# Kernel optimization log

Measured on AMD Instinct MI355X. Metric: run time of the kernel, lower is better.

Reference implementation:

```python
import jax, jax.numpy as jnp
import numpy as np

B, C, H, W = 16, 3, 512, 512
NUM_BANDS = 100


def setup_inputs() -> dict:
    key = jax.random.key(0)
    k1, k2, k3 = jax.random.split(key, 3)
    clean = jax.random.normal(k1, (B, C, H, W), dtype=jnp.float32)
    noisy = jax.random.normal(k2, (B, C, H, W), dtype=jnp.float32)
    # value_prob = arange(1.0, 0.0, -0.01) * 0.3, bernoulli per batch row
    probs = (1.0 - 0.01 * jnp.arange(NUM_BANDS, dtype=jnp.float32)) * 0.3  # (100,)
    value_set = jax.random.bernoulli(k3, probs[None, :].repeat(B, axis=0)).astype(jnp.float32)  # (B,100)
    return {"clean": clean, "noisy": noisy, "value_set": value_set}


def reference(clean, noisy, value_set):
    b, c, h, w = noisy.shape
    # radial distance map from image center (meshgrid 'ij' as in torch)
    a = jnp.arange(h, dtype=jnp.float32)[:, None]
    bb = jnp.arange(w, dtype=jnp.float32)[None, :]
    dist = jnp.sqrt((a - h / 2) ** 2 + (bb - w / 2) ** 2)  # (H,W)
    max_radius = float(np.sqrt(h * h + w * w) / 2)
    radius_set = max_radius * jnp.arange(0.01, 1.01, 0.01, dtype=jnp.float32)  # (100,)

    # FFT + full fftshift (torch default shifts ALL axes, incl. batch/channel)
    noisy_fq = jnp.fft.fftshift(jnp.fft.fftn(noisy, axes=(-1, -2)))
    clean_fq = jnp.fft.fftshift(jnp.fft.fftn(clean, axes=(-1, -2)))

    # Fused bucketize + gather replacing the 100-iteration mask loop:
    # band i covers radius_set[i-1] <= dist < radius_set[i]  ->  searchsorted right
    idx = jnp.searchsorted(radius_set, dist, side='right')  # (H,W), values in [0,100]
    in_range = idx < radius_set.shape[0]
    idx_c = jnp.minimum(idx, radius_set.shape[0] - 1)
    bn1_mask = jnp.where(in_range[None, :, :], value_set[:, idx_c], 0.0)  # (B,H,W)
    bn2_mask = 1.0 - bn1_mask

    replaced_fq = noisy_fq * bn1_mask[:, None, :, :] + clean_fq * bn2_mask[:, None, :, :]
    replaced_fq = jnp.fft.ifftshift(replaced_fq)
    out = jnp.fft.ifftn(replaced_fq, axes=(-1, -2))
    return out.real
```

## Files before the change

### kernel.cpp

```cpp
#include <hip/hip_runtime.h>
#include <math.h>


using cplx = float2;

__device__ __forceinline__ cplx cmul(cplx a, cplx b){
  return make_float2(a.x*b.x - a.y*b.y, a.x*b.y + a.y*b.x);
}
__device__ __forceinline__ cplx cadd(cplx a, cplx b){ return make_float2(a.x+b.x, a.y+b.y); }
__device__ __forceinline__ cplx csub(cplx a, cplx b){ return make_float2(a.x-b.x, a.y-b.y); }
template<int S> __device__ __forceinline__ cplx muli(cplx a){
  return (S < 0) ? make_float2(a.y, -a.x) : make_float2(-a.y, a.x);
}
__device__ __forceinline__ int sw(int i){ return i ^ (((i >> 6) & 7) << 1); }

template<int S>
__device__ __forceinline__ void dft8(cplx v[8]){
  const float R2 = 0.70710678118654752440f;
  cplx e0 = cadd(v[0], v[4]), e1 = csub(v[0], v[4]);
  cplx o0 = cadd(v[2], v[6]), o1 = muli<S>(csub(v[2], v[6]));
  cplx E0 = cadd(e0, o0), E1 = cadd(e1, o1), E2 = csub(e0, o0), E3 = csub(e1, o1);
  cplx f0 = cadd(v[1], v[5]), f1 = csub(v[1], v[5]);
  cplx g0 = cadd(v[3], v[7]), g1 = muli<S>(csub(v[3], v[7]));
  cplx F0 = cadd(f0, g0), F1 = cadd(f1, g1), F2 = csub(f0, g0), F3 = csub(f1, g1);
  const cplx w1 = make_float2( R2, (float)S * R2);
  const cplx w3 = make_float2(-R2, (float)S * R2);
  cplx t0 = F0, t1 = cmul(w1, F1), t2 = muli<S>(F2), t3 = cmul(w3, F3);
  v[0] = cadd(E0, t0); v[4] = csub(E0, t0);
  v[1] = cadd(E1, t1); v[5] = csub(E1, t1);
  v[2] = cadd(E2, t2); v[6] = csub(E2, t2);
  v[3] = cadd(E3, t3); v[7] = csub(E3, t3);
}

template<int S>
__device__ __forceinline__ void twiddle8_pair(cplx a[8], cplx b[8], float ang){
  float sn, c_; __sincosf(ang, &sn, &c_);
  cplx w = make_float2(c_, sn), cur = w;
  #pragma unroll
  for(int r = 1; r < 8; r++){ a[r] = cmul(a[r], cur); b[r] = cmul(b[r], cur); cur = cmul(cur, w); }
}

template<int S, int STR>
__device__ __forceinline__ void fft512_pair(cplx a[8], cplx b[8], cplx* sa, cplx* sb, int t){
  const float PI2 = 6.283185307179586f;
  dft8<S>(a); dft8<S>(b);
  #pragma unroll
  for(int r = 0; r < 8; r++){ int i = sw(t*8 + r)*STR; sa[i] = a[r]; sb[i] = b[r]; }
  #pragma unroll
  for(int r = 0; r < 8; r++){ int i = sw(t + 64*r)*STR; a[r] = sa[i]; b[r] = sb[i]; }
  twiddle8_pair<S>(a, b, (float)S * PI2 * (1.0f/64.0f) * (float)(t & 7));
  dft8<S>(a); dft8<S>(b);
  int d1 = ((t >> 3) << 6) | (t & 7);
  #pragma unroll
  for(int r = 0; r < 8; r++){ int i = sw(d1 + (r << 3))*STR; sa[i] = a[r]; sb[i] = b[r]; }
  #pragma unroll
  for(int r = 0; r < 8; r++){ int i = sw(t + 64*r)*STR; a[r] = sa[i]; b[r] = sb[i]; }
  twiddle8_pair<S>(a, b, (float)S * PI2 * (1.0f/512.0f) * (float)t);
  dft8<S>(a); dft8<S>(b);
}

__device__ __forceinline__ void packed_images(int p, int& i0, int& i1, int& b1, int& b2){
  if (p < 16){ i0 = 3*p; i1 = 3*p + 1; b1 = p; b2 = p; }
  else { int q = p - 16; i0 = 6*q + 2; i1 = 6*q + 5; b1 = 2*q; b2 = 2*q + 1; }
}

__device__ __forceinline__ int slot_col(int s, int j){
  int c = (j < 4) ? (4*s + j) : (505 - 4*s + j);
  c &= 511;
  if (s == 0 && j == 7) c = 256;
  return c;
}

__global__ __launch_bounds__(256) void k_rowfft(const float* __restrict__ noisy,
                                                const float* __restrict__ clean,
                                                float2* __restrict__ ws){
  __shared__ cplx scr[8][512];
  int blk = blockIdx.x;
  int p = blk >> 6, h8 = (blk & 63) << 3;
  int i0, i1, b1, b2; packed_images(p, i0, i1, b1, b2);
  const float* n0 = noisy + (size_t)i0 * 262144;
  const float* c0 = clean + (size_t)i0 * 262144;
  const float* n1 = noisy + (size_t)i1 * 262144;
  const float* c1 = clean + (size_t)i1 * 262144;
  int wid = threadIdx.x >> 6, t = threadIdx.x & 63;
  int hA = h8 + wid*2, hB = hA + 1;
  cplx a[8], b[8];
  #pragma unroll
  for(int r = 0; r < 8; r++){
    int iA = hA*512 + t + 64*r;
    int iB = hB*512 + t + 64*r;
    a[r] = make_float2(n0[iA]-c0[iA], n1[iA]-c1[iA]);
    b[r] = make_float2(n0[iB]-c0[iB], n1[iB]-c1[iB]);
  }
  fft512_pair<-1,1>(a, b, scr[wid*2], scr[wid*2+1], t);
  float2* oA = ws + (size_t)p*262144 + hA*512;
  float2* oB = ws + (size_t)p*262144 + hB*512;
  #pragma unroll
  for(int r = 0; r < 8; r++){ oA[t+64*r] = a[r]; oB[t+64*r] = b[r]; }
}

#define INV_BAND 0.27621358640099513f

__global__ __launch_bounds__(256) void k_colfft(float2* __restrict__ ws,
                                                const float* __restrict__ value_set){
  __shared__ cplx tile[512][9];
  int blk = blockIdx.x;
  int p = blk >> 6, s = blk & 63;
  int i0, i1, b1, b2; packed_images(p, i0, i1, b1, b2);
  const float* vs1 = value_set + ((b1 + 8) & 15) * 100;
  const float* vs2 = value_set + ((b2 + 8) & 15) * 100;
  float2* base = ws + (size_t)p * 262144;
  int tid = threadIdx.x;

  {
    int j = tid & 7, cj = slot_col(s, j);
    #pragma unroll
    for(int h0 = 0; h0 < 512; h0 += 32){
      int h = h0 + (tid >> 3);
      tile[h][j] = base[h*512 + cj];
    }
  }
  __syncthreads();

  int wid = tid >> 6, t = tid & 63;
  int sA = wid, sB = 7 - wid;
  int colA = slot_col(s, sA);
  int colB = slot_col(s, sB);
  int fwA = (colA < 256) ? colA : colA - 512;
  int fwB = (colB < 256) ? colB : colB - 512;
  int fw2A = fwA * fwA;
  int fw2B = fwB * fwB;
  bool selfp = (s == 0 && wid == 0);
  int pA = selfp ? sA : sB;
  int pB = selfp ? sB : sA;

  cplx a[8], b[8];
  #pragma unroll
  for(int r = 0; r < 8; r++){ a[r] = tile[t+64*r][sA]; b[r] = tile[t+64*r][sB]; }
  fft512_pair<-1,9>(a, b, &tile[0][sA], &tile[0][sB], t);
  #pragma unroll
  for(int r = 0; r < 8; r++){ tile[t+64*r][sA] = a[r]; tile[t+64*r][sB] = b[r]; }
  #pragma unroll
  for(int r = 0; r < 8; r++){
    int h = t + 64*r;
    int fh = (h < 256) ? h : h - 512;
    int fh2 = fh * fh;
    float rrA = sqrtf((float)(fh2 + fw2A));
    float rrB = sqrtf((float)(fh2 + fw2B));
    int bandA = (int)(rrA * INV_BAND);
    int bandB = (int)(rrB * INV_BAND);
    float m1A = (bandA < 100) ? vs1[bandA] : 0.0f;
    float m2A = (bandA < 100) ? vs2[bandA] : 0.0f;
    float m1B = (bandB < 100) ? vs1[bandB] : 0.0f;
    float m2B = (bandB < 100) ? vs2[bandB] : 0.0f;
    float csA = 0.5f*(m1A + m2A) * (1.0f/262144.0f);
    float cdA = 0.5f*(m1A - m2A) * (1.0f/262144.0f);
    float csB = 0.5f*(m1B + m2B) * (1.0f/262144.0f);
    float cdB = 0.5f*(m1B - m2B) * (1.0f/262144.0f);
    int ph = (512 - h) & 511;
    float2 PA = tile[ph][pA];
    float2 PB = tile[ph][pB];
    cplx na = make_float2(csA*a[r].x + cdA*PA.x, csA*a[r].y - cdA*PA.y);
    cplx nb = make_float2(csB*b[r].x + cdB*PB.x, csB*b[r].y - cdB*PB.y);
    a[r] = na; b[r] = nb;
  }
  fft512_pair<1,9>(a, b, &tile[0][sA], &tile[0][sB], t);
  #pragma unroll
  for(int r = 0; r < 8; r++){ tile[t+64*r][sA] = a[r]; tile[t+64*r][sB] = b[r]; }
  __syncthreads();

  {
    int j = tid & 7, cj = slot_col(s, j);
    #pragma unroll
    for(int h0 = 0; h0 < 512; h0 += 32){
      int h = h0 + (tid >> 3);
      base[h*512 + cj] = tile[h][j];
    }
  }
}

__global__ __launch_bounds__(256) void k_rowifft(const float2* __restrict__ ws,
                                                 const float* __restrict__ clean,
                                                 float* __restrict__ out){
  __shared__ cplx scr[8][512];
  int blk = blockIdx.x;
  int p = blk >> 6, h8 = (blk & 63) << 3;
  int i0, i1, b1, b2; packed_images(p, i0, i1, b1, b2);
  int wid = threadIdx.x >> 6, t = threadIdx.x & 63;
  int hA = h8 + wid*2, hB = hA + 1;
  const float2* iA_ = ws + (size_t)p*262144 + hA*512;
  const float2* iB_ = ws + (size_t)p*262144 + hB*512;
  cplx a[8], b[8];
  #pragma unroll
  for(int r = 0; r < 8; r++){ a[r] = iA_[t+64*r]; b[r] = iB_[t+64*r]; }
  fft512_pair<1,1>(a, b, scr[wid*2], scr[wid*2+1], t);
  const float* c0 = clean + (size_t)i0 * 262144;
  const float* c1 = clean + (size_t)i1 * 262144;
  float* o0 = out + (size_t)i0 * 262144;
  float* o1 = out + (size_t)i1 * 262144;
  #pragma unroll
  for(int r = 0; r < 8; r++){
    int iA = hA*512 + t + 64*r;
    int iB = hB*512 + t + 64*r;
    o0[iA] = a[r].x + c0[iA];
    o1[iA] = a[r].y + c1[iA];
    o0[iB] = b[r].x + c0[iB];
    o1[iB] = b[r].y + c1[iB];
  }
}

extern "C" void kernel_launch(void* const* d_in, const int* in_sizes, int n_in,
                              void* d_out, int out_size, void* d_ws, size_t ws_size,
                              hipStream_t stream){
  const float* clean     = (const float*)d_in[0];
  const float* noisy     = (const float*)d_in[1];
  const float* value_set = (const float*)d_in[2];
  float* out = (float*)d_out;
  float2* ws = (float2*)d_ws;

  k_rowfft <<<1536, 256, 0, stream>>>(noisy, clean, ws);
  k_colfft <<<1536, 256, 0, stream>>>(ws, value_set);
  k_rowifft<<<1536, 256, 0, stream>>>(ws, clean, out);
}
```

Before: 227.8 us.

## Fold conjugate column pairs adjacent in workspace and widen column FFT tiles

The row FFT now writes each row in a folded order, so column w and its conjugate partner 512-w sit next to each other, and the row IFFT reads back with the same mapping. The column kernel can then load 16 contiguous columns per block (512 threads, 768 blocks) instead of gathering 8 scattered columns, which makes the global loads and stores contiguous. The shared tile uses an XOR-swizzled layout to avoid bank conflicts. Packed images from the same batch skip the conjugate-partner read and extra tile store in the mask step. The row kernels also get an occupancy hint in launch_bounds. The change risks higher register pressure in the larger column blocks and a new, more complex index mapping that has to be correct.

```diff
diff --git a/kernel.cpp b/kernel.cpp
--- a/kernel.cpp
+++ b/kernel.cpp
@@ -13,6 +13,11 @@
   return (S < 0) ? make_float2(a.y, -a.x) : make_float2(-a.y, a.x);
 }
 __device__ __forceinline__ int sw(int i){ return i ^ (((i >> 6) & 7) << 1); }
+#define ADDR(i,j) (((i) << 4) + ((j) ^ ((((i) >> 3) ^ (((i) & 7) << 1)) & 15)))
+
+__device__ __forceinline__ int fold(int w){
+  return (w < 256) ? 2*w : ((w == 256) ? 1 : 2*(512 - w) + 1);
+}
 
 template<int S>
 __device__ __forceinline__ void dft8(cplx v[8]){
@@ -40,21 +45,40 @@
   for(int r = 1; r < 8; r++){ a[r] = cmul(a[r], cur); b[r] = cmul(b[r], cur); cur = cmul(cur, w); }
 }
 
-template<int S, int STR>
+template<int S>
 __device__ __forceinline__ void fft512_pair(cplx a[8], cplx b[8], cplx* sa, cplx* sb, int t){
   const float PI2 = 6.283185307179586f;
   dft8<S>(a); dft8<S>(b);
   #pragma unroll
-  for(int r = 0; r < 8; r++){ int i = sw(t*8 + r)*STR; sa[i] = a[r]; sb[i] = b[r]; }
-  #pragma unroll
-  for(int r = 0; r < 8; r++){ int i = sw(t + 64*r)*STR; a[r] = sa[i]; b[r] = sb[i]; }
+  for(int r = 0; r < 8; r++){ int i = sw(t*8 + r); sa[i] = a[r]; sb[i] = b[r]; }
+  #pragma unroll
+  for(int r = 0; r < 8; r++){ int i = sw(t + 64*r); a[r] = sa[i]; b[r] = sb[i]; }
   twiddle8_pair<S>(a, b, (float)S * PI2 * (1.0f/64.0f) * (float)(t & 7));
   dft8<S>(a); dft8<S>(b);
   int d1 = ((t >> 3) << 6) | (t & 7);
   #pragma unroll
-  for(int r = 0; r < 8; r++){ int i = sw(d1 + (r << 3))*STR; sa[i] = a[r]; sb[i] = b[r]; }
-  #pragma unroll
-  for(int r = 0; r < 8; r++){ int i = sw(t + 64*r)*STR; a[r] = sa[i]; b[r] = sb[i]; }
+  for(int r = 0; r < 8; r++){ int i = sw(d1 + (r << 3)); sa[i] = a[r]; sb[i] = b[r]; }
+  #pragma unroll
+  for(int r = 0; r < 8; r++){ int i = sw(t + 64*r); a[r] = sa[i]; b[r] = sb[i]; }
+  twiddle8_pair<S>(a, b, (float)S * PI2 * (1.0f/512.0f) * (float)t);
+  dft8<S>(a); dft8<S>(b);
+}
+
+template<int S>
+__device__ __forceinline__ void fft512_pair_tile(cplx a[8], cplx b[8], cplx* T, int jA, int jB, int t){
+  const float PI2 = 6.283185307179586f;
+  dft8<S>(a); dft8<S>(b);
+  #pragma unroll
+  for(int r = 0; r < 8; r++){ int i = t*8 + r; T[ADDR(i,jA)] = a[r]; T[ADDR(i,jB)] = b[r]; }
+  #pragma unroll
+  for(int r = 0; r < 8; r++){ int i = t + 64*r; a[r] = T[ADDR(i,jA)]; b[r] = T[ADDR(i,jB)]; }
+  twiddle8_pair<S>(a, b, (float)S * PI2 * (1.0f/64.0f) * (float)(t & 7));
+  dft8<S>(a); dft8<S>(b);
+  int d1 = ((t >> 3) << 6) | (t & 7);
+  #pragma unroll
+  for(int r = 0; r < 8; r++){ int i = d1 + (r << 3); T[ADDR(i,jA)] = a[r]; T[ADDR(i,jB)] = b[r]; }
+  #pragma unroll
+  for(int r = 0; r < 8; r++){ int i = t + 64*r; a[r] = T[ADDR(i,jA)]; b[r] = T[ADDR(i,jB)]; }
   twiddle8_pair<S>(a, b, (float)S * PI2 * (1.0f/512.0f) * (float)t);
   dft8<S>(a); dft8<S>(b);
 }
@@ -64,16 +88,9 @@
   else { int q = p - 16; i0 = 6*q + 2; i1 = 6*q + 5; b1 = 2*q; b2 = 2*q + 1; }
 }
 
-__device__ __forceinline__ int slot_col(int s, int j){
-  int c = (j < 4) ? (4*s + j) : (505 - 4*s + j);
-  c &= 511;
-  if (s == 0 && j == 7) c = 256;
-  return c;
-}
-
-__global__ __launch_bounds__(256) void k_rowfft(const float* __restrict__ noisy,
-                                                const float* __restrict__ clean,
-                                                float2* __restrict__ ws){
+__global__ __launch_bounds__(256, 5) void k_rowfft(const float* __restrict__ noisy,
+                                                   const float* __restrict__ clean,
+                                                   float2* __restrict__ ws){
   __shared__ cplx scr[8][512];
   int blk = blockIdx.x;
   int p = blk >> 6, h8 = (blk & 63) << 3;
@@ -92,96 +109,114 @@
     a[r] = make_float2(n0[iA]-c0[iA], n1[iA]-c1[iA]);
     b[r] = make_float2(n0[iB]-c0[iB], n1[iB]-c1[iB]);
   }
-  fft512_pair<-1,1>(a, b, scr[wid*2], scr[wid*2+1], t);
+  fft512_pair<-1>(a, b, scr[wid*2], scr[wid*2+1], t);
   float2* oA = ws + (size_t)p*262144 + hA*512;
   float2* oB = ws + (size_t)p*262144 + hB*512;
   #pragma unroll
-  for(int r = 0; r < 8; r++){ oA[t+64*r] = a[r]; oB[t+64*r] = b[r]; }
+  for(int r = 0; r < 8; r++){
+    int s = fold(t + 64*r);
+    oA[s] = a[r]; oB[s] = b[r];
+  }
 }
 
 #define INV_BAND 0.27621358640099513f
 
-__global__ __launch_bounds__(256) void k_colfft(float2* __restrict__ ws,
+__global__ __launch_bounds__(512) void k_colfft(float2* __restrict__ ws,
                                                 const float* __restrict__ value_set){
-  __shared__ cplx tile[512][9];
+  __shared__ cplx tile[512 * 16];
   int blk = blockIdx.x;
-  int p = blk >> 6, s = blk & 63;
+  int p = blk >> 5, m = blk & 31;
   int i0, i1, b1, b2; packed_images(p, i0, i1, b1, b2);
   const float* vs1 = value_set + ((b1 + 8) & 15) * 100;
   const float* vs2 = value_set + ((b2 + 8) & 15) * 100;
-  float2* base = ws + (size_t)p * 262144;
+  bool cross = (p >= 16);
+  float2* base = ws + (size_t)p * 262144 + 16*m;
   int tid = threadIdx.x;
 
   {
-    int j = tid & 7, cj = slot_col(s, j);
+    int j = tid & 15, hb = tid >> 4;
     #pragma unroll
     for(int h0 = 0; h0 < 512; h0 += 32){
-      int h = h0 + (tid >> 3);
-      tile[h][j] = base[h*512 + cj];
+      int h = h0 + hb;
+      tile[ADDR(h, j)] = base[(size_t)h * 512 + j];
     }
   }
   __syncthreads();
 
   int wid = tid >> 6, t = tid & 63;
-  int sA = wid, sB = 7 - wid;
-  int colA = slot_col(s, sA);
-  int colB = slot_col(s, sB);
-  int fwA = (colA < 256) ? colA : colA - 512;
-  int fwB = (colB < 256) ? colB : colB - 512;
-  int fw2A = fwA * fwA;
-  int fw2B = fwB * fwB;
-  bool selfp = (s == 0 && wid == 0);
-  int pA = selfp ? sA : sB;
-  int pB = selfp ? sB : sA;
+  int jA = wid*2, jB = wid*2 + 1;
+  int SA = 16*m + jA;
+  int wA = SA >> 1;
+  int fw2A = wA * wA;
+  int fw2B = (SA == 0) ? 65536 : wA * wA;
+  bool selfp = (SA == 0);
+  int pjA = selfp ? jA : jB;
+  int pjB = selfp ? jB : jA;
 
   cplx a[8], b[8];
   #pragma unroll
-  for(int r = 0; r < 8; r++){ a[r] = tile[t+64*r][sA]; b[r] = tile[t+64*r][sB]; }
-  fft512_pair<-1,9>(a, b, &tile[0][sA], &tile[0][sB], t);
-  #pragma unroll
-  for(int r = 0; r < 8; r++){ tile[t+64*r][sA] = a[r]; tile[t+64*r][sB] = b[r]; }
-  #pragma unroll
-  for(int r = 0; r < 8; r++){
-    int h = t + 64*r;
-    int fh = (h < 256) ? h : h - 512;
-    int fh2 = fh * fh;
-    float rrA = sqrtf((float)(fh2 + fw2A));
-    float rrB = sqrtf((float)(fh2 + fw2B));
-    int bandA = (int)(rrA * INV_BAND);
-    int bandB = (int)(rrB * INV_BAND);
-    float m1A = (bandA < 100) ? vs1[bandA] : 0.0f;
-    float m2A = (bandA < 100) ? vs2[bandA] : 0.0f;
-    float m1B = (bandB < 100) ? vs1[bandB] : 0.0f;
-    float m2B = (bandB < 100) ? vs2[bandB] : 0.0f;
-    float csA = 0.5f*(m1A + m2A) * (1.0f/262144.0f);
-    float cdA = 0.5f*(m1A - m2A) * (1.0f/262144.0f);
-    float csB = 0.5f*(m1B + m2B) * (1.0f/262144.0f);
-    float cdB = 0.5f*(m1B - m2B) * (1.0f/262144.0f);
-    int ph = (512 - h) & 511;
-    float2 PA = tile[ph][pA];
-    float2 PB = tile[ph][pB];
-    cplx na = make_float2(csA*a[r].x + cdA*PA.x, csA*a[r].y - cdA*PA.y);
-    cplx nb = make_float2(csB*b[r].x + cdB*PB.x, csB*b[r].y - cdB*PB.y);
-    a[r] = na; b[r] = nb;
-  }
-  fft512_pair<1,9>(a, b, &tile[0][sA], &tile[0][sB], t);
-  #pragma unroll
-  for(int r = 0; r < 8; r++){ tile[t+64*r][sA] = a[r]; tile[t+64*r][sB] = b[r]; }
+  for(int r = 0; r < 8; r++){ int i = t + 64*r; a[r] = tile[ADDR(i,jA)]; b[r] = tile[ADDR(i,jB)]; }
+  fft512_pair_tile<-1>(a, b, tile, jA, jB, t);
+
+  if (cross){
+    #pragma unroll
+    for(int r = 0; r < 8; r++){ int i = t + 64*r; tile[ADDR(i,jA)] = a[r]; tile[ADDR(i,jB)] = b[r]; }
+    #pragma unroll
+    for(int r = 0; r < 8; r++){
+      int h = t + 64*r;
+      int fh = (h < 256) ? h : h - 512;
+      int fh2 = fh * fh;
+      int bandA = (int)(sqrtf((float)(fh2 + fw2A)) * INV_BAND);
+      int bandB = (int)(sqrtf((float)(fh2 + fw2B)) * INV_BAND);
+      float m1A = (bandA < 100) ? vs1[bandA] : 0.0f;
+      float m2A = (bandA < 100) ? vs2[bandA] : 0.0f;
+      float m1B = (bandB < 100) ? vs1[bandB] : 0.0f;
+      float m2B = (bandB < 100) ? vs2[bandB] : 0.0f;
+      float csA = 0.5f*(m1A + m2A) * (1.0f/262144.0f);
+      float cdA = 0.5f*(m1A - m2A) * (1.0f/262144.0f);
+      float csB = 0.5f*(m1B + m2B) * (1.0f/262144.0f);
+      float cdB = 0.5f*(m1B - m2B) * (1.0f/262144.0f);
+      int ph = (512 - h) & 511;
+      float2 PA = tile[ADDR(ph, pjA)];
+      float2 PB = tile[ADDR(ph, pjB)];
+      a[r] = make_float2(csA*a[r].x + cdA*PA.x, csA*a[r].y - cdA*PA.y);
+      b[r] = make_float2(csB*b[r].x + cdB*PB.x, csB*b[r].y - cdB*PB.y);
+    }
+  } else {
+    #pragma unroll
+    for(int r = 0; r < 8; r++){
+      int h = t + 64*r;
+      int fh = (h < 256) ? h : h - 512;
+      int fh2 = fh * fh;
+      int bandA = (int)(sqrtf((float)(fh2 + fw2A)) * INV_BAND);
+      int bandB = (int)(sqrtf((float)(fh2 + fw2B)) * INV_BAND);
+      float mA = (bandA < 100) ? vs1[bandA] : 0.0f;
+      float mB = (bandB < 100) ? vs1[bandB] : 0.0f;
+      float csA = mA * (1.0f/262144.0f);
+      float csB = mB * (1.0f/262144.0f);
+      a[r].x *= csA; a[r].y *= csA;
+      b[r].x *= csB; b[r].y *= csB;
+    }
+  }
+
+  fft512_pair_tile<1>(a, b, tile, jA, jB, t);
+  #pragma unroll
+  for(int r = 0; r < 8; r++){ int i = t + 64*r; tile[ADDR(i,jA)] = a[r]; tile[ADDR(i,jB)] = b[r]; }
   __syncthreads();
 
   {
-    int j = tid & 7, cj = slot_col(s, j);
+    int j = tid & 15, hb = tid >> 4;
     #pragma unroll
     for(int h0 = 0; h0 < 512; h0 += 32){
-      int h = h0 + (tid >> 3);
-      base[h*512 + cj] = tile[h][j];
-    }
-  }
-}
-
-__global__ __launch_bounds__(256) void k_rowifft(const float2* __restrict__ ws,
-                                                 const float* __restrict__ clean,
-                                                 float* __restrict__ out){
+      int h = h0 + hb;
+      base[(size_t)h * 512 + j] = tile[ADDR(h, j)];
+    }
+  }
+}
+
+__global__ __launch_bounds__(256, 5) void k_rowifft(const float2* __restrict__ ws,
+                                                    const float* __restrict__ clean,
+                                                    float* __restrict__ out){
   __shared__ cplx scr[8][512];
   int blk = blockIdx.x;
   int p = blk >> 6, h8 = (blk & 63) << 3;
@@ -192,8 +227,11 @@
   const float2* iB_ = ws + (size_t)p*262144 + hB*512;
   cplx a[8], b[8];
   #pragma unroll
-  for(int r = 0; r < 8; r++){ a[r] = iA_[t+64*r]; b[r] = iB_[t+64*r]; }
-  fft512_pair<1,1>(a, b, scr[wid*2], scr[wid*2+1], t);
+  for(int r = 0; r < 8; r++){
+    int s = fold(t + 64*r);
+    a[r] = iA_[s]; b[r] = iB_[s];
+  }
+  fft512_pair<1>(a, b, scr[wid*2], scr[wid*2+1], t);
   const float* c0 = clean + (size_t)i0 * 262144;
   const float* c1 = clean + (size_t)i1 * 262144;
   float* o0 = out + (size_t)i0 * 262144;
@@ -219,6 +257,6 @@
   float2* ws = (float2*)d_ws;
 
   k_rowfft <<<1536, 256, 0, stream>>>(noisy, clean, ws);
-  k_colfft <<<1536, 256, 0, stream>>>(ws, value_set);
+  k_colfft <<< 768, 512, 0, stream>>>(ws, value_set);
   k_rowifft<<<1536, 256, 0, stream>>>(ws, clean, out);
 }
```

Result: faster. 206.1 us (-9.5%).
